# Optimization experiments

Measured on AMD Instinct MI355X. Metric: run time of the kernel, lower is better.

Reference implementation:

```python
import jax, jax.numpy as jnp
import numpy as np

EPS = 1e-5  # BatchNorm eps; fresh module eval => running_mean=0, running_var=1


def _cbr(t, W, g, b):
    # 1x1 conv (no bias) over [B,C,L] + BatchNorm2d(eval, mean0/var1) + ReLU
    t = jnp.einsum('oc,bcl->bol', W, t)
    t = t * (g / jnp.sqrt(1.0 + EPS))[None, :, None] + b[None, :, None]
    return jax.nn.relu(t)


def _wavelet(y):
    # SFP.wavelet: chunk channels into 3; for chunk i (1-based) take the level-i
    # haar wavedec approximation coeffs along axis 2 and mean-reduce them.
    # For even lengths, level-i haar approx = block-sum over 2^i samples * 2^(-i/2).
    B, C, L = y.shape
    parts = jnp.split(y, 3, axis=1)
    zs = []
    for i, k in enumerate(parts, start=1):
        s = 2 ** i
        a = k.reshape(B, C // 3, L // s, s).sum(-1) * (2.0 ** (-i / 2))  # [B,C/3,L/2^i]
        zs.append(a.mean(axis=2))
    return jnp.concatenate(zs, axis=1)  # [B,C]


def setup_inputs() -> dict:
    key = jax.random.key(0)
    ks = jax.random.split(key, 16)
    B, C, H, W = 32, 384, 64, 64
    R = C // 16
    f = lambda k, sh, s=0.05: jax.random.normal(k, sh, jnp.float32) * s
    u = lambda k, sh: jax.random.uniform(k, sh, jnp.float32, 0.5, 1.5)
    return dict(
        x=jax.random.normal(ks[0], (B, C, H, W), jnp.float32),
        Wy=f(ks[1], (C, C)), gy=u(ks[2], (C,)), by=f(ks[3], (C,)),
        Wh=f(ks[4], (C, C)), gh=u(ks[5], (C,)), bh=f(ks[6], (C,)),
        Ww=f(ks[7], (C, C)), gw=u(ks[8], (C,)), bw=f(ks[9], (C,)),
        fc0_w=f(ks[10], (R, C)), fc0_b=f(ks[11], (R,)),
        bn1_g=u(ks[12], (R,)), bn1_b=f(ks[13], (R,)),
        fc1_w=f(ks[14], (C, R)), fc1_b=f(ks[15], (C,)),
    )


def reference(x, Wy, gy, by, Wh, gh, bh, Ww, gw, bw,
              fc0_w, fc0_b, bn1_g, bn1_b, fc1_w, fc1_b):
    B, C, H, Wd = x.shape
    # CoordPooling: mean over width -> [B,C,H]; mean over height -> [B,C,W]; cat along coord axis
    y = jnp.concatenate([x.mean(axis=3), x.mean(axis=2)], axis=2)  # [B,C,H+W]
    y = _cbr(y, Wy, gy, by)
    xh = _cbr(y[:, :, :H], Wh, gh, bh)   # [B,C,H]
    xw = _cbr(y[:, :, H:], Ww, gw, bw)   # [B,C,W]
    # SFP channel gate (torch detaches y before the wavelet)
    z = _wavelet(jax.lax.stop_gradient(y))          # [B,C]
    z = z @ fc0_w.T + fc0_b                          # [B,C/16]
    z = jax.nn.relu(z * (bn1_g / jnp.sqrt(1.0 + EPS)) + bn1_b)
    z = z @ fc1_w.T + fc1_b                          # [B,C]
    gate = jax.nn.sigmoid(xh[:, :, :, None] * xw[:, :, None, :])  # [B,C,H,W]
    return x * gate + x * z[:, :, None, None]
```

## Files before the change

### kernel.cpp

```cpp
#include <hip/hip_runtime.h>
#include <math.h>

#define RSQ 0.99999500003749975f

typedef __attribute__((ext_vector_type(8))) __bf16 bf16x8;
typedef __attribute__((ext_vector_type(4))) float f32x4;
typedef __attribute__((ext_vector_type(4))) unsigned int u32x4;
typedef __attribute__((ext_vector_type(2))) unsigned int u32x2;

__device__ __forceinline__ unsigned short bfb(float v) {
    return __builtin_bit_cast(unsigned short, (__bf16)v);
}
__device__ __forceinline__ float bff(unsigned short u) {
    unsigned int x = ((unsigned int)u) << 16;
    return __builtin_bit_cast(float, x);
}

__global__ __launch_bounds__(256) void kpool(const float* __restrict__ x,
                                             const float* __restrict__ Wy,
                                             const float* __restrict__ Wh,
                                             const float* __restrict__ Ww,
                                             unsigned short* __restrict__ ypb,
                                             unsigned short* __restrict__ Wp) {
    __shared__ float sm[6208];
    int bid = blockIdx.x;
    int t = threadIdx.x;
    if (bid >= 12288) {
        int e = bid - 12288;
        int m = e / 24, ot = e % 24;
        const float* W = (m == 0) ? Wy : (m == 1) ? Wh : Ww;
#pragma unroll
        for (int k = 0; k < 6; ++k) {
            int idx = t + k * 256;
            int r = idx / 96, c4 = idx % 96;
            f32x4 v = *reinterpret_cast<const f32x4*>(W + (size_t)(ot * 16 + r) * 384 + c4 * 4);
            *reinterpret_cast<f32x4*>(&sm[r * 388 + c4 * 4]) = v;
        }
        __syncthreads();
#pragma unroll
        for (int k = 0; k < 3; ++k) {
            int idx = t + k * 256;
            int cs = idx >> 6, j = idx & 63;
            const float* src = &sm[(j & 15) * 388 + cs * 32 + (j >> 4) * 8];
            u32x4 pk;
            pk.x = (unsigned int)bfb(src[0]) | ((unsigned int)bfb(src[1]) << 16);
            pk.y = (unsigned int)bfb(src[2]) | ((unsigned int)bfb(src[3]) << 16);
            pk.z = (unsigned int)bfb(src[4]) | ((unsigned int)bfb(src[5]) << 16);
            pk.w = (unsigned int)bfb(src[6]) | ((unsigned int)bfb(src[7]) << 16);
            *reinterpret_cast<u32x4*>(Wp + ((size_t)(m * 24 + ot) * 12 + cs) * 512 + j * 8) = pk;
        }
        return;
    }
    float* pl = sm;
    float* part = sm + 4096;
    const f32x4* xp = reinterpret_cast<const f32x4*>(x) + (size_t)bid * 1024;
    f32x4* pl4 = reinterpret_cast<f32x4*>(pl);
#pragma unroll
    for (int k = 0; k < 4; ++k) pl4[k * 256 + t] = __builtin_nontemporal_load(xp + k * 256 + t);
    __syncthreads();
    int lane = t & 63, pt = t >> 6;
    float rs = 0.f;
#pragma unroll
    for (int j = 0; j < 16; ++j) {
        int w = (pt * 16 + j + lane) & 63;
        rs += pl[lane * 64 + w];
    }
    part[t] = rs;
    __syncthreads();
    if (t < 64) {
        float v = part[t] + part[t + 64] + part[t + 128] + part[t + 192];
        ypb[(size_t)bid * 128 + t] = bfb(v * 0.015625f);
    }
    __syncthreads();
    float cs = 0.f;
#pragma unroll
    for (int j = 0; j < 16; ++j) cs += pl[(pt * 16 + j) * 64 + lane];
    part[t] = cs;
    __syncthreads();
    if (t < 64) {
        float v = part[t] + part[t + 64] + part[t + 128] + part[t + 192];
        ypb[(size_t)bid * 128 + 64 + t] = bfb(v * 0.015625f);
    }
}

__global__ __launch_bounds__(256) void kcbr(const unsigned short* __restrict__ in16,
    const unsigned short* __restrict__ Wp,
    const float* __restrict__ g0, const float* __restrict__ b0,
    const float* __restrict__ g1, const float* __restrict__ b1,
    int m_lo, int m_hi,
    unsigned short* __restrict__ outb, float* __restrict__ outf,
    const float* __restrict__ fc0_w, const float* __restrict__ fc0_b,
    const float* __restrict__ bn1_g, const float* __restrict__ bn1_b,
    const float* __restrict__ fc1_w, const float* __restrict__ fc1_b,
    float* __restrict__ z2) {
    int bid = blockIdx.x;
    int t = threadIdx.x;
    if (bid >= 768) {
        __shared__ float z0[384];
        __shared__ float z1[24];
        int b = bid - 768;
        const unsigned short* yb = in16 + (size_t)b * 49152;
        for (int c = t; c < 384; c += 256) {
            const u32x4* r4 = reinterpret_cast<const u32x4*>(yb + (size_t)c * 128);
            float s = 0.f;
#pragma unroll
            for (int j = 0; j < 16; ++j) {
                u32x4 v = r4[j];
                s += bff((unsigned short)(v.x & 0xffff)) + bff((unsigned short)(v.x >> 16));
                s += bff((unsigned short)(v.y & 0xffff)) + bff((unsigned short)(v.y >> 16));
                s += bff((unsigned short)(v.z & 0xffff)) + bff((unsigned short)(v.z >> 16));
                s += bff((unsigned short)(v.w & 0xffff)) + bff((unsigned short)(v.w >> 16));
            }
            float fac = (c < 128) ? 1.41421356237310f : (c < 256 ? 2.0f : 2.82842712474619f);
            z0[c] = s * (fac * 0.0078125f);
        }
        __syncthreads();
        if (t < 96) {
            int r = t >> 2, j = t & 3;
            float p = 0.f;
            for (int c = j; c < 384; c += 4) p = fmaf(z0[c], fc0_w[r * 384 + c], p);
            p += __shfl_xor(p, 1);
            p += __shfl_xor(p, 2);
            if (j == 0) z1[r] = fmaxf(fmaf(p + fc0_b[r], bn1_g[r] * RSQ, bn1_b[r]), 0.f);
        }
        __syncthreads();
        for (int c = t; c < 384; c += 256) {
            float a = fc1_b[c];
#pragma unroll
            for (int r = 0; r < 24; ++r) a = fmaf(z1[r], fc1_w[c * 24 + r], a);
            z2[b * 384 + c] = a;
        }
        return;
    }
    __shared__ unsigned short As[2048];
    __shared__ unsigned short Bs[1024];
    int ot = bid % 6;
    int lt = (bid / 6) % 4;
    int b  = bid / 24;
    int o0 = ot * 64, l0 = lt * 32;
    int m = (lt >= 2) ? m_hi : m_lo;
    const float* g  = (lt >= 2) ? g1 : g0;
    const float* bb = (lt >= 2) ? b1 : b0;
    int w = t >> 6, lane = t & 63;
    const unsigned short* Asrc = Wp + ((size_t)(m * 24 + ot * 4 + w) * 12) * 512 + (size_t)lane * 8;
    int cB = t >> 3, l4 = (t & 7) * 4;
    const unsigned short* Bsrc = in16 + (size_t)b * 49152 + (size_t)cB * 128 + l0 + l4;
    unsigned short* BsW = &Bs[(cB >> 3) * 256 + (cB & 7)];

    u32x4 ar = *reinterpret_cast<const u32x4*>(Asrc);
    u32x2 br = *reinterpret_cast<const u32x2*>(Bsrc);
    f32x4 acc0 = {0.f, 0.f, 0.f, 0.f};
    f32x4 acc1 = {0.f, 0.f, 0.f, 0.f};

    for (int ch = 0; ch < 12; ++ch) {
        if (ch) __syncthreads();
        *reinterpret_cast<u32x4*>(&As[t * 8]) = ar;
        BsW[(l4 + 0) * 8] = (unsigned short)(br.x & 0xffff);
        BsW[(l4 + 1) * 8] = (unsigned short)(br.x >> 16);
        BsW[(l4 + 2) * 8] = (unsigned short)(br.y & 0xffff);
        BsW[(l4 + 3) * 8] = (unsigned short)(br.y >> 16);
        __syncthreads();
        if (ch < 11) {
            ar = *reinterpret_cast<const u32x4*>(Asrc + (ch + 1) * 512);
            br = *reinterpret_cast<const u32x2*>(Bsrc + (ch + 1) * 4096);
        }
        bf16x8 av  = *reinterpret_cast<const bf16x8*>(&As[w * 512 + lane * 8]);
        bf16x8 bv0 = *reinterpret_cast<const bf16x8*>(&Bs[(lane >> 4) * 256 + (lane & 15) * 8]);
        bf16x8 bv1 = *reinterpret_cast<const bf16x8*>(&Bs[(lane >> 4) * 256 + 128 + (lane & 15) * 8]);
        acc0 = __builtin_amdgcn_mfma_f32_16x16x32_bf16(av, bv0, acc0, 0, 0, 0);
        acc1 = __builtin_amdgcn_mfma_f32_16x16x32_bf16(av, bv1, acc1, 0, 0, 0);
    }
    int oB = o0 + w * 16 + (lane >> 4) * 4;
    int lB = l0 + (lane & 15);
    if (outb) {
#pragma unroll
        for (int r = 0; r < 4; ++r) {
            int o = oB + r;
            float sc = g[o] * RSQ, bi = bb[o];
            size_t base = ((size_t)b * 384 + o) * 128 + lB;
            outb[base]      = bfb(fmaxf(fmaf(acc0[r], sc, bi), 0.f));
            outb[base + 16] = bfb(fmaxf(fmaf(acc1[r], sc, bi), 0.f));
        }
    } else {
#pragma unroll
        for (int r = 0; r < 4; ++r) {
            int o = oB + r;
            float sc = g[o] * RSQ, bi = bb[o];
            size_t base = ((size_t)b * 384 + o) * 128 + lB;
            outf[base]      = fmaxf(fmaf(acc0[r], sc, bi), 0.f);
            outf[base + 16] = fmaxf(fmaf(acc1[r], sc, bi), 0.f);
        }
    }
}

__global__ __launch_bounds__(256) void kfinal(const float* __restrict__ x,
    const float* __restrict__ hw, const float* __restrict__ z2,
    float* __restrict__ out) {
    const f32x4* x4 = reinterpret_cast<const f32x4*>(x);
    f32x4* o4 = reinterpret_cast<f32x4*>(out);
    const int total4 = 12582912;
    int stride = gridDim.x * blockDim.x;
    for (int idx = blockIdx.x * blockDim.x + threadIdx.x; idx < total4; idx += stride) {
        int w4 = idx & 15;
        int h  = (idx >> 4) & 63;
        int bc = idx >> 10;
        f32x4 xv = __builtin_nontemporal_load(x4 + idx);
        float  a  = hw[(bc << 7) + h];
        const f32x4 wv = reinterpret_cast<const f32x4*>(hw)[(bc << 5) + 16 + w4];
        float  zv = z2[bc];
        f32x4 ov;
        ov.x = xv.x * (1.f / (1.f + __expf(-a * wv.x)) + zv);
        ov.y = xv.y * (1.f / (1.f + __expf(-a * wv.y)) + zv);
        ov.z = xv.z * (1.f / (1.f + __expf(-a * wv.z)) + zv);
        ov.w = xv.w * (1.f / (1.f + __expf(-a * wv.w)) + zv);
        __builtin_nontemporal_store(ov, o4 + idx);
    }
}

extern "C" void kernel_launch(void* const* d_in, const int* in_sizes, int n_in,
                              void* d_out, int out_size, void* d_ws, size_t ws_size,
                              hipStream_t stream) {
    const float* x     = (const float*)d_in[0];
    const float* Wy    = (const float*)d_in[1];
    const float* gy    = (const float*)d_in[2];
    const float* by    = (const float*)d_in[3];
    const float* Wh    = (const float*)d_in[4];
    const float* gh    = (const float*)d_in[5];
    const float* bh    = (const float*)d_in[6];
    const float* Ww    = (const float*)d_in[7];
    const float* gw    = (const float*)d_in[8];
    const float* bw    = (const float*)d_in[9];
    const float* fc0_w = (const float*)d_in[10];
    const float* fc0_b = (const float*)d_in[11];
    const float* bn1_g = (const float*)d_in[12];
    const float* bn1_b = (const float*)d_in[13];
    const float* fc1_w = (const float*)d_in[14];
    const float* fc1_b = (const float*)d_in[15];
    float* out = (float*)d_out;

    char* ws = (char*)d_ws;
    unsigned short* ypb = (unsigned short*)ws;
    unsigned short* yb  = (unsigned short*)(ws + 3145728);
    float*          hw  = (float*)(ws + 6291456);
    float*          z2  = (float*)(ws + 12582912);
    unsigned short* Wp  = (unsigned short*)(ws + 12632064);

    kpool<<<dim3(12288 + 72), dim3(256), 0, stream>>>(x, Wy, Wh, Ww, ypb, Wp);
    kcbr<<<dim3(768), dim3(256), 0, stream>>>(ypb, Wp, gy, by, gy, by, 0, 0, yb, nullptr,
        fc0_w, fc0_b, bn1_g, bn1_b, fc1_w, fc1_b, z2);
    kcbr<<<dim3(800), dim3(256), 0, stream>>>(yb, Wp, gh, bh, gw, bw, 1, 2, nullptr, hw,
        fc0_w, fc0_b, bn1_g, bn1_b, fc1_w, fc1_b, z2);
    kfinal<<<dim3(2048), dim3(256), 0, stream>>>(x, hw, z2, out);
}
```

Before: 138.2 us.

## Split CBR kernel, store intermediate y transposed, read MFMA operands directly

The single templated CBR kernel is split into two. The first GEMM stages B through double-buffered shared memory and reads A straight from global, then writes its bf16 output transposed as [B,L,C]. The second GEMM, and the wavelet reduction fused with it, read this transposed layout directly from global with no shared-memory staging or barriers. The aim is to remove LDS round trips and syncs in these small GEMMs. The cost is a transposed store and a reduction loop in the gate path that now walks 128 strided rows serially.

```diff
diff --git a/kernel.cpp b/kernel.cpp
--- a/kernel.cpp
+++ b/kernel.cpp
@@ -83,12 +83,86 @@
     }
 }
 
-__global__ __launch_bounds__(256) void kcbr(const unsigned short* __restrict__ in16,
+__global__ __launch_bounds__(256) void kcbr1(const unsigned short* __restrict__ yp,
     const unsigned short* __restrict__ Wp,
-    const float* __restrict__ g0, const float* __restrict__ b0,
-    const float* __restrict__ g1, const float* __restrict__ b1,
-    int m_lo, int m_hi,
-    unsigned short* __restrict__ outb, float* __restrict__ outf,
+    const float* __restrict__ g, const float* __restrict__ bb,
+    unsigned short* __restrict__ yT) {
+    __shared__ unsigned short Bs[2][2048];
+    int bid = blockIdx.x;
+    int t = threadIdx.x;
+    int ot = bid % 6, lt = (bid / 6) % 4, b = bid / 24;
+    int o0 = ot * 64, l0 = lt * 32;
+    int w = t >> 6, lane = t & 63;
+
+    int c_s0 = t >> 3,            l4_0 = (t & 7) * 4;
+    int c_s1 = (t + 256) >> 3,    l4_1 = l4_0;
+    const unsigned short* ypbase = yp + (size_t)b * 49152 + l0;
+    const unsigned short* Asrc = Wp + (size_t)(ot * 4 + w) * 12 * 512 + lane * 8;
+
+    f32x4 acc0 = {0.f, 0.f, 0.f, 0.f};
+    f32x4 acc1 = {0.f, 0.f, 0.f, 0.f};
+
+    auto stage = [&](int buf, u32x2 r0, u32x2 r1) {
+        unsigned short* B0 = &Bs[buf][(c_s0 >> 3) * 256 + l4_0 * 8 + (c_s0 & 7)];
+        B0[0]  = (unsigned short)(r0.x & 0xffff);
+        B0[8]  = (unsigned short)(r0.x >> 16);
+        B0[16] = (unsigned short)(r0.y & 0xffff);
+        B0[24] = (unsigned short)(r0.y >> 16);
+        unsigned short* B1 = &Bs[buf][(c_s1 >> 3) * 256 + l4_1 * 8 + (c_s1 & 7)];
+        B1[0]  = (unsigned short)(r1.x & 0xffff);
+        B1[8]  = (unsigned short)(r1.x >> 16);
+        B1[16] = (unsigned short)(r1.y & 0xffff);
+        B1[24] = (unsigned short)(r1.y >> 16);
+    };
+    auto ldB = [&](int ch, u32x2& r0, u32x2& r1) {
+        r0 = *reinterpret_cast<const u32x2*>(ypbase + (size_t)(ch * 64 + c_s0) * 128 + l4_0);
+        r1 = *reinterpret_cast<const u32x2*>(ypbase + (size_t)(ch * 64 + c_s1) * 128 + l4_1);
+    };
+
+    u32x2 r0, r1;
+    ldB(0, r0, r1);
+    stage(0, r0, r1);
+#pragma unroll
+    for (int ch = 0; ch < 6; ++ch) {
+        __syncthreads();
+        if (ch < 5) ldB(ch + 1, r0, r1);
+        const unsigned short* Bb = Bs[ch & 1];
+        int li = lane & 15, hi = lane >> 4;
+#pragma unroll
+        for (int kk = 0; kk < 2; ++kk) {
+            bf16x8 av = *reinterpret_cast<const bf16x8*>(Asrc + (size_t)(ch * 2 + kk) * 512);
+            int cg = kk * 4 + hi;
+            bf16x8 bv0 = *reinterpret_cast<const bf16x8*>(&Bb[cg * 256 + li * 8]);
+            bf16x8 bv1 = *reinterpret_cast<const bf16x8*>(&Bb[cg * 256 + (li + 16) * 8]);
+            acc0 = __builtin_amdgcn_mfma_f32_16x16x32_bf16(av, bv0, acc0, 0, 0, 0);
+            acc1 = __builtin_amdgcn_mfma_f32_16x16x32_bf16(av, bv1, acc1, 0, 0, 0);
+        }
+        if (ch < 5) stage((ch + 1) & 1, r0, r1);
+    }
+    int oB = o0 + w * 16 + (lane >> 4) * 4;
+    int lB = l0 + (lane & 15);
+    float s0 = g[oB] * RSQ,     bi0 = bb[oB];
+    float s1 = g[oB + 1] * RSQ, bi1 = bb[oB + 1];
+    float s2 = g[oB + 2] * RSQ, bi2 = bb[oB + 2];
+    float s3 = g[oB + 3] * RSQ, bi3 = bb[oB + 3];
+    u32x2 p0, p1;
+    p0.x = (unsigned int)bfb(fmaxf(fmaf(acc0[0], s0, bi0), 0.f)) |
+           ((unsigned int)bfb(fmaxf(fmaf(acc0[1], s1, bi1), 0.f)) << 16);
+    p0.y = (unsigned int)bfb(fmaxf(fmaf(acc0[2], s2, bi2), 0.f)) |
+           ((unsigned int)bfb(fmaxf(fmaf(acc0[3], s3, bi3), 0.f)) << 16);
+    p1.x = (unsigned int)bfb(fmaxf(fmaf(acc1[0], s0, bi0), 0.f)) |
+           ((unsigned int)bfb(fmaxf(fmaf(acc1[1], s1, bi1), 0.f)) << 16);
+    p1.y = (unsigned int)bfb(fmaxf(fmaf(acc1[2], s2, bi2), 0.f)) |
+           ((unsigned int)bfb(fmaxf(fmaf(acc1[3], s3, bi3), 0.f)) << 16);
+    *reinterpret_cast<u32x2*>(yT + ((size_t)b * 128 + lB) * 384 + oB) = p0;
+    *reinterpret_cast<u32x2*>(yT + ((size_t)b * 128 + lB + 16) * 384 + oB) = p1;
+}
+
+__global__ __launch_bounds__(256) void kcbr2(const unsigned short* __restrict__ yT,
+    const unsigned short* __restrict__ Wp,
+    const float* __restrict__ gh, const float* __restrict__ bh,
+    const float* __restrict__ gw, const float* __restrict__ bw,
+    float* __restrict__ hw,
     const float* __restrict__ fc0_w, const float* __restrict__ fc0_b,
     const float* __restrict__ bn1_g, const float* __restrict__ bn1_b,
     const float* __restrict__ fc1_w, const float* __restrict__ fc1_b,
@@ -99,20 +173,16 @@
         __shared__ float z0[384];
         __shared__ float z1[24];
         int b = bid - 768;
-        const unsigned short* yb = in16 + (size_t)b * 49152;
-        for (int c = t; c < 384; c += 256) {
-            const u32x4* r4 = reinterpret_cast<const u32x4*>(yb + (size_t)c * 128);
-            float s = 0.f;
-#pragma unroll
-            for (int j = 0; j < 16; ++j) {
-                u32x4 v = r4[j];
-                s += bff((unsigned short)(v.x & 0xffff)) + bff((unsigned short)(v.x >> 16));
-                s += bff((unsigned short)(v.y & 0xffff)) + bff((unsigned short)(v.y >> 16));
-                s += bff((unsigned short)(v.z & 0xffff)) + bff((unsigned short)(v.z >> 16));
-                s += bff((unsigned short)(v.w & 0xffff)) + bff((unsigned short)(v.w >> 16));
-            }
-            float fac = (c < 128) ? 1.41421356237310f : (c < 256 ? 2.0f : 2.82842712474619f);
-            z0[c] = s * (fac * 0.0078125f);
+        const unsigned short* yb = yT + (size_t)b * 49152;
+        float sA = 0.f, sB = 0.f;
+        for (int l = 0; l < 128; ++l) {
+            sA += bff(yb[l * 384 + t]);
+            if (t < 128) sB += bff(yb[l * 384 + 256 + t]);
+        }
+        {
+            float facA = (t < 128) ? 1.41421356237310f : 2.0f;
+            z0[t] = sA * (facA * 0.0078125f);
+            if (t < 128) z0[256 + t] = sB * (2.82842712474619f * 0.0078125f);
         }
         __syncthreads();
         if (t < 96) {
@@ -132,64 +202,36 @@
         }
         return;
     }
-    __shared__ unsigned short As[2048];
-    __shared__ unsigned short Bs[1024];
-    int ot = bid % 6;
-    int lt = (bid / 6) % 4;
-    int b  = bid / 24;
+    int ot = bid % 6, lt = (bid / 6) % 4, b = bid / 24;
     int o0 = ot * 64, l0 = lt * 32;
-    int m = (lt >= 2) ? m_hi : m_lo;
-    const float* g  = (lt >= 2) ? g1 : g0;
-    const float* bb = (lt >= 2) ? b1 : b0;
+    int m = (lt >= 2) ? 2 : 1;
+    const float* g  = (lt >= 2) ? gw : gh;
+    const float* bb = (lt >= 2) ? bw : bh;
     int w = t >> 6, lane = t & 63;
-    const unsigned short* Asrc = Wp + ((size_t)(m * 24 + ot * 4 + w) * 12) * 512 + (size_t)lane * 8;
-    int cB = t >> 3, l4 = (t & 7) * 4;
-    const unsigned short* Bsrc = in16 + (size_t)b * 49152 + (size_t)cB * 128 + l0 + l4;
-    unsigned short* BsW = &Bs[(cB >> 3) * 256 + (cB & 7)];
-
-    u32x4 ar = *reinterpret_cast<const u32x4*>(Asrc);
-    u32x2 br = *reinterpret_cast<const u32x2*>(Bsrc);
+    int li = lane & 15, hi = lane >> 4;
+    const unsigned short* Asrc = Wp + (size_t)(m * 24 + ot * 4 + w) * 12 * 512 + lane * 8;
+    const unsigned short* B0 = yT + ((size_t)b * 128 + l0 + li) * 384 + hi * 8;
+    const unsigned short* B1 = B0 + (size_t)16 * 384;
+
     f32x4 acc0 = {0.f, 0.f, 0.f, 0.f};
     f32x4 acc1 = {0.f, 0.f, 0.f, 0.f};
-
+#pragma unroll
     for (int ch = 0; ch < 12; ++ch) {
-        if (ch) __syncthreads();
-        *reinterpret_cast<u32x4*>(&As[t * 8]) = ar;
-        BsW[(l4 + 0) * 8] = (unsigned short)(br.x & 0xffff);
-        BsW[(l4 + 1) * 8] = (unsigned short)(br.x >> 16);
-        BsW[(l4 + 2) * 8] = (unsigned short)(br.y & 0xffff);
-        BsW[(l4 + 3) * 8] = (unsigned short)(br.y >> 16);
-        __syncthreads();
-        if (ch < 11) {
-            ar = *reinterpret_cast<const u32x4*>(Asrc + (ch + 1) * 512);
-            br = *reinterpret_cast<const u32x2*>(Bsrc + (ch + 1) * 4096);
-        }
-        bf16x8 av  = *reinterpret_cast<const bf16x8*>(&As[w * 512 + lane * 8]);
-        bf16x8 bv0 = *reinterpret_cast<const bf16x8*>(&Bs[(lane >> 4) * 256 + (lane & 15) * 8]);
-        bf16x8 bv1 = *reinterpret_cast<const bf16x8*>(&Bs[(lane >> 4) * 256 + 128 + (lane & 15) * 8]);
+        bf16x8 av  = *reinterpret_cast<const bf16x8*>(Asrc + (size_t)ch * 512);
+        bf16x8 bv0 = *reinterpret_cast<const bf16x8*>(B0 + ch * 32);
+        bf16x8 bv1 = *reinterpret_cast<const bf16x8*>(B1 + ch * 32);
         acc0 = __builtin_amdgcn_mfma_f32_16x16x32_bf16(av, bv0, acc0, 0, 0, 0);
         acc1 = __builtin_amdgcn_mfma_f32_16x16x32_bf16(av, bv1, acc1, 0, 0, 0);
     }
-    int oB = o0 + w * 16 + (lane >> 4) * 4;
-    int lB = l0 + (lane & 15);
-    if (outb) {
-#pragma unroll
-        for (int r = 0; r < 4; ++r) {
-            int o = oB + r;
-            float sc = g[o] * RSQ, bi = bb[o];
-            size_t base = ((size_t)b * 384 + o) * 128 + lB;
-            outb[base]      = bfb(fmaxf(fmaf(acc0[r], sc, bi), 0.f));
-            outb[base + 16] = bfb(fmaxf(fmaf(acc1[r], sc, bi), 0.f));
-        }
-    } else {
-#pragma unroll
-        for (int r = 0; r < 4; ++r) {
-            int o = oB + r;
-            float sc = g[o] * RSQ, bi = bb[o];
-            size_t base = ((size_t)b * 384 + o) * 128 + lB;
-            outf[base]      = fmaxf(fmaf(acc0[r], sc, bi), 0.f);
-            outf[base + 16] = fmaxf(fmaf(acc1[r], sc, bi), 0.f);
-        }
+    int oB = o0 + w * 16 + hi * 4;
+    int lB = l0 + li;
+#pragma unroll
+    for (int r = 0; r < 4; ++r) {
+        int o = oB + r;
+        float sc = g[o] * RSQ, bi = bb[o];
+        size_t base = ((size_t)b * 384 + o) * 128 + lB;
+        hw[base]      = fmaxf(fmaf(acc0[r], sc, bi), 0.f);
+        hw[base + 16] = fmaxf(fmaf(acc1[r], sc, bi), 0.f);
     }
 }
 
@@ -240,15 +282,14 @@
 
     char* ws = (char*)d_ws;
     unsigned short* ypb = (unsigned short*)ws;
-    unsigned short* yb  = (unsigned short*)(ws + 3145728);
+    unsigned short* yT  = (unsigned short*)(ws + 3145728);
     float*          hw  = (float*)(ws + 6291456);
     float*          z2  = (float*)(ws + 12582912);
     unsigned short* Wp  = (unsigned short*)(ws + 12632064);
 
     kpool<<<dim3(12288 + 72), dim3(256), 0, stream>>>(x, Wy, Wh, Ww, ypb, Wp);
-    kcbr<<<dim3(768), dim3(256), 0, stream>>>(ypb, Wp, gy, by, gy, by, 0, 0, yb, nullptr,
-        fc0_w, fc0_b, bn1_g, bn1_b, fc1_w, fc1_b, z2);
-    kcbr<<<dim3(800), dim3(256), 0, stream>>>(yb, Wp, gh, bh, gw, bw, 1, 2, nullptr, hw,
+    kcbr1<<<dim3(768), dim3(256), 0, stream>>>(ypb, Wp, gy, by, yT);
+    kcbr2<<<dim3(800), dim3(256), 0, stream>>>(yT, Wp, gh, bh, gw, bw, hw,
         fc0_w, fc0_b, bn1_g, bn1_b, fc1_w, fc1_b, z2);
     kfinal<<<dim3(2048), dim3(256), 0, stream>>>(x, hw, z2, out);
 }
```

After: 156.7 us. 13.4% more time.
